# Kernel optimization log

Measured on AMD Instinct MI355X. Metric: run time of the kernel, lower is better.

The kernel has to match this reference:

```python
import jax, jax.numpy as jnp
import numpy as np

BITS = 4
MAXQ = 15          # (1 << BITS) - 1
PACK = 32 // BITS  # 8 values packed per int32


def dequantize(qweight, qzeros, scales, g_idx):
    """GPTQ 4-bit dequant. qweight: [K//8, N] int32, qzeros: [G, N//8] int32,
    scales: [G, N] float, g_idx: [K] int32 -> dense W [K, N] float."""
    N = qweight.shape[1]
    shifts = (jnp.arange(PACK, dtype=jnp.uint32) * BITS)  # [8]
    qw = qweight.astype(jnp.uint32)
    # unpack along K: k = row*8 + j  (matches shifter = (k % 8) * bits)
    w_int = ((qw[:, None, :] >> shifts[None, :, None]) & MAXQ).reshape(-1, N)  # [K, N]
    qz = qzeros.astype(jnp.uint32)
    # unpack along N: n = col*8 + j  (matches zeros_shifter = (n % 8) * bits)
    z_int = ((qz[:, :, None] >> shifts[None, None, :]) & MAXQ).reshape(qzeros.shape[0], -1) + 1  # [G, N]
    dt = scales.dtype
    # group-wise dequant: w = (q - zero) * scale, gathered per-row via g_idx
    return (w_int.astype(dt) - z_int[g_idx].astype(dt)) * scales[g_idx]


def setup_inputs() -> dict:
    key = jax.random.key(0)
    k1, k2, k3, k4, k5 = jax.random.split(key, 5)
    M, K, N, GS = 128, 4096, 11008, 128
    G = K // GS
    x = jax.random.normal(k1, (M, K), dtype=jnp.float32)
    qweight = jax.random.randint(k2, (K // PACK, N), 0, 2147483647, dtype=jnp.int32)
    qzeros = jax.random.randint(k3, (G, N // PACK), 0, 2147483647, dtype=jnp.int32)
    scales = jax.random.uniform(k4, (G, N), dtype=jnp.float32, minval=0.001, maxval=0.01)
    bias = jax.random.normal(k5, (N,), dtype=jnp.float32)
    g_idx = (jnp.arange(K, dtype=jnp.int32) // GS).astype(jnp.int32)
    return {"x": x, "qweight": qweight, "qzeros": qzeros, "scales": scales,
            "bias": bias, "g_idx": g_idx}


def reference(x, qweight, qzeros, scales, bias, g_idx):
    w = dequantize(qweight, qzeros, scales, g_idx)  # [K, N]
    return x @ w + bias
```

## Files before the change

kernel.cpp:

```cpp
#include <hip/hip_runtime.h>
#include <stdint.h>


#define M_DIM 128
#define K_DIM 4096
#define N_DIM 11008
#define GS    128
#define NG    32
#define SPLIT 4
#define GPB   (NG / SPLIT)
#define PART_STRIDE ((size_t)M_DIM * N_DIM)

typedef _Float16 half8  __attribute__((ext_vector_type(8)));
typedef _Float16 half2t __attribute__((ext_vector_type(2)));
typedef _Float16 half4t __attribute__((ext_vector_type(4)));
typedef float    f32x4  __attribute__((ext_vector_type(4)));

__global__ void k_prep(const float* __restrict__ x, const int* __restrict__ qzeros,
                       const float* __restrict__ scales,
                       _Float16* __restrict__ xh, float* __restrict__ zs) {
    int b = blockIdx.x, tid = threadIdx.x;
    if (b < 512) {
        int i = (b * 256 + tid) * 4;
        float4 v = *(const float4*)(x + i);
        half4t o;
        o[0] = (_Float16)v.x; o[1] = (_Float16)v.y;
        o[2] = (_Float16)v.z; o[3] = (_Float16)v.w;
        *(half4t*)(xh + i) = o;
    } else {
        b -= 512;
        int g = b / 43;
        int n = (b - g * 43) * 256 + tid;
        unsigned qz = (unsigned)qzeros[g * (N_DIM / 8) + (n >> 3)];
        float z = (float)((qz >> ((n & 7) * 4)) & 15u) + 1.0f;
        zs[g * N_DIM + n] = z * scales[g * N_DIM + n];
    }
}

__device__ __forceinline__ void load_lds16(const void* g, void* l) {
    __builtin_amdgcn_global_load_lds(
        (const __attribute__((address_space(1))) unsigned int*)g,
        (__attribute__((address_space(3))) unsigned int*)l, 16, 0, 0);
}

__device__ __forceinline__ half8 dequant8(unsigned q, half2t S2, half2t Z2) {
    const half2t BIAS = __builtin_bit_cast(half2t, 0x64006400u);
    half2t w[4];
#pragma unroll
    for (int p = 0; p < 4; ++p) {
        unsigned r = __builtin_amdgcn_perm(q, q, 0x00010001u * (unsigned)p);
        unsigned t = (r & 0x00F0000Fu) | 0x64006400u;
        w[p] = __builtin_elementwise_fma(__builtin_bit_cast(half2t, t) - BIAS, S2, Z2);
    }
    half4t lo = __builtin_shufflevector(w[0], w[1], 0, 1, 2, 3);
    half4t hi = __builtin_shufflevector(w[2], w[3], 0, 1, 2, 3);
    return __builtin_shufflevector(lo, hi, 0, 1, 2, 3, 4, 5, 6, 7);
}

__global__ __launch_bounds__(512, 4)
void k_gemm(const _Float16* __restrict__ xh,
            const int*      __restrict__ qweight,
            const float*    __restrict__ scales,
            const float*    __restrict__ zst,
            float*          __restrict__ part)
{
    __shared__ _Float16 As[2][128 * 128];

    const int tid  = threadIdx.x;
    const int lane = tid & 63;
    const int w    = tid >> 6;
    const int wx   = w & 1;
    const int wy   = (w >> 1) & 1;
    const int kh   = w >> 2;
    const int q    = lane >> 4;
    const int lr   = lane & 15;

    const int n0 = blockIdx.x * 64;
    const int g0 = blockIdx.y * GPB;
    int ncol[2] = { n0 + wx * 32 + lr, n0 + wx * 32 + lr + 16 };

    f32x4 acc[4][2];
#pragma unroll
    for (int f = 0; f < 4; ++f)
#pragma unroll
        for (int h = 0; h < 2; ++h)
            acc[f][h] = (f32x4){0.f, 0.f, 0.f, 0.f};

    int cm[4], ckb[4];
#pragma unroll
    for (int it = 0; it < 4; ++it) {
        int c = it * 512 + tid;
        cm[it]  = c >> 4;
        ckb[it] = (c & 15) ^ (cm[it] & 15);
    }
    const int wave_lds = w * 64 * 8;

#pragma unroll
    for (int it = 0; it < 4; ++it)
        load_lds16(xh + (size_t)cm[it] * K_DIM + g0 * GS + ckb[it] * 8,
                   &As[0][it * 512 * 8 + wave_lds]);
    unsigned qwn[4];
    float scn[2], zcn[2];
#pragma unroll
    for (int t = 0; t < 2; ++t)
#pragma unroll
        for (int h = 0; h < 2; ++h)
            qwn[t * 2 + h] = (unsigned)qweight[(size_t)(g0 * 16 + (kh * 2 + t) * 4 + q) * N_DIM + ncol[h]];
#pragma unroll
    for (int h = 0; h < 2; ++h) {
        scn[h] = scales[(size_t)g0 * N_DIM + ncol[h]];
        zcn[h] = zst[(size_t)g0 * N_DIM + ncol[h]];
    }

    int p = 0;
    for (int g = 0; g < GPB; ++g) {
        unsigned qw[4];
        float sc[2], zc[2];
#pragma unroll
        for (int i = 0; i < 4; ++i) qw[i] = qwn[i];
#pragma unroll
        for (int h = 0; h < 2; ++h) { sc[h] = scn[h]; zc[h] = zcn[h]; }

        __syncthreads();

        if (g + 1 < GPB) {
            int gn = g0 + g + 1;
#pragma unroll
            for (int it = 0; it < 4; ++it)
                load_lds16(xh + (size_t)cm[it] * K_DIM + gn * GS + ckb[it] * 8,
                           &As[p ^ 1][it * 512 * 8 + wave_lds]);
#pragma unroll
            for (int t = 0; t < 2; ++t)
#pragma unroll
                for (int h = 0; h < 2; ++h)
                    qwn[t * 2 + h] = (unsigned)qweight[(size_t)(gn * 16 + (kh * 2 + t) * 4 + q) * N_DIM + ncol[h]];
#pragma unroll
            for (int h = 0; h < 2; ++h) {
                scn[h] = scales[(size_t)gn * N_DIM + ncol[h]];
                zcn[h] = zst[(size_t)gn * N_DIM + ncol[h]];
            }
        }

        half2t S2[2], Z2[2];
#pragma unroll
        for (int h = 0; h < 2; ++h) {
            float s = sc[h], z1 = zc[h];
            S2[h][0] = (_Float16)s;
            S2[h][1] = (_Float16)(s * 0.0625f);
            Z2[h][0] = (_Float16)(-z1);
            Z2[h][1] = (_Float16)(-z1);
        }

#pragma unroll
        for (int t = 0; t < 2; ++t) {
            const int kk = kh * 2 + t;
            half8 bf[2];
#pragma unroll
            for (int h = 0; h < 2; ++h)
                bf[h] = dequant8(qw[t * 2 + h], S2[h], Z2[h]);
#pragma unroll
            for (int f = 0; f < 4; ++f) {
                int m   = wy * 64 + f * 16 + lr;
                int kb2 = (kk * 4 + q) ^ lr;
                half8 af = *(const half8*)(&As[p][m * 128 + kb2 * 8]);
#pragma unroll
                for (int h = 0; h < 2; ++h)
                    acc[f][h] = __builtin_amdgcn_mfma_f32_16x16x32_f16(af, bf[h], acc[f][h], 0, 0, 0);
            }
        }
        p ^= 1;
    }

    __syncthreads();
    float* red = (float*)&As[0][0];
    const int pid = w & 3;
    if (w >= 4) {
#pragma unroll
        for (int f = 0; f < 4; ++f)
#pragma unroll
            for (int h = 0; h < 2; ++h)
                *(f32x4*)(red + pid * 2048 + (f * 2 + h) * 256 + lane * 4) = acc[f][h];
    }
    __syncthreads();
    if (w < 4) {
        float* po = part + (size_t)blockIdx.y * PART_STRIDE;
#pragma unroll
        for (int f = 0; f < 4; ++f) {
            int mrow = wy * 64 + f * 16 + q * 4;
#pragma unroll
            for (int h = 0; h < 2; ++h) {
                f32x4 o = acc[f][h] + *(const f32x4*)(red + pid * 2048 + (f * 2 + h) * 256 + lane * 4);
#pragma unroll
                for (int r = 0; r < 4; ++r)
                    po[(size_t)(mrow + r) * N_DIM + ncol[h]] = o[r];
            }
        }
    }
}

__global__ void k_reduce(const float* __restrict__ part, const float* __restrict__ bias,
                         float* __restrict__ out) {
    int i = (blockIdx.x * 256 + threadIdx.x) * 4;
    int m = i / N_DIM;
    int n = i - m * N_DIM;
    f32x4 s = *(const f32x4*)(bias + n);
#pragma unroll
    for (int sp = 0; sp < SPLIT; ++sp)
        s += *(const f32x4*)(part + sp * PART_STRIDE + i);
    *(f32x4*)(out + i) = s;
}

extern "C" void kernel_launch(void* const* d_in, const int* in_sizes, int n_in,
                              void* d_out, int out_size, void* d_ws, size_t ws_size,
                              hipStream_t stream) {
    const float* x       = (const float*)d_in[0];
    const int*   qweight = (const int*)d_in[1];
    const int*   qzeros  = (const int*)d_in[2];
    const float* scales  = (const float*)d_in[3];
    const float* bias    = (const float*)d_in[4];

    char* ws = (char*)d_ws;
    _Float16* xh   = (_Float16*)ws;
    float*    zst  = (float*)(ws + 1048576);
    float*    part = (float*)(ws + 1048576 + 1409024);

    k_prep  <<<dim3(1888),            dim3(256), 0, stream>>>(x, qzeros, scales, xh, zst);
    k_gemm  <<<dim3(N_DIM/64, SPLIT), dim3(512), 0, stream>>>(xh, qweight, scales, zst, part);
    k_reduce<<<dim3(1376),            dim3(256), 0, stream>>>(part, bias, (float*)d_out);
}
```

Before: 106.5 us.

## Pack fp16 scale/zero pairs and store split-K partials as fp16 fragment tiles

The prep kernel now writes one packed half4 per column holding scale, scale/16 and the negated zero*scale. This replaces the two separate fp32 scale and zero loads in the GEMM with a single 8-byte load and removes the in-loop conversions. Split-K partials are stored in fp16 in MFMA fragment order with contiguous half4 writes rather than scattered fp32 row stores. The reduce kernel reads that layout and does the row scatter itself. Partial traffic is halved, but the rounding of partial sums to fp16 costs accuracy.

```diff
diff --git a/kernel.cpp b/kernel.cpp
--- a/kernel.cpp
+++ b/kernel.cpp
@@ -9,7 +9,8 @@
 #define NG    32
 #define SPLIT 4
 #define GPB   (NG / SPLIT)
-#define PART_STRIDE ((size_t)M_DIM * N_DIM)
+#define NB    (N_DIM / 64)
+#define PART_ELEMS ((size_t)NB * 4 * 2048)
 
 typedef _Float16 half8  __attribute__((ext_vector_type(8)));
 typedef _Float16 half2t __attribute__((ext_vector_type(2)));
@@ -18,7 +19,7 @@
 
 __global__ void k_prep(const float* __restrict__ x, const int* __restrict__ qzeros,
                        const float* __restrict__ scales,
-                       _Float16* __restrict__ xh, float* __restrict__ zs) {
+                       _Float16* __restrict__ xh, _Float16* __restrict__ szp) {
     int b = blockIdx.x, tid = threadIdx.x;
     if (b < 512) {
         int i = (b * 256 + tid) * 4;
@@ -32,8 +33,14 @@
         int g = b / 43;
         int n = (b - g * 43) * 256 + tid;
         unsigned qz = (unsigned)qzeros[g * (N_DIM / 8) + (n >> 3)];
-        float z = (float)((qz >> ((n & 7) * 4)) & 15u) + 1.0f;
-        zs[g * N_DIM + n] = z * scales[g * N_DIM + n];
+        float s  = scales[g * N_DIM + n];
+        float z1 = (float)((qz >> ((n & 7) * 4)) & 15u) + 1.0f;
+        half4t o;
+        o[0] = (_Float16)s;
+        o[1] = (_Float16)(s * 0.0625f);
+        o[2] = (_Float16)(-(z1 * s));
+        o[3] = o[2];
+        *(half4t*)(szp + (size_t)(g * N_DIM + n) * 4) = o;
     }
 }
 
@@ -60,9 +67,8 @@
 __global__ __launch_bounds__(512, 4)
 void k_gemm(const _Float16* __restrict__ xh,
             const int*      __restrict__ qweight,
-            const float*    __restrict__ scales,
-            const float*    __restrict__ zst,
-            float*          __restrict__ part)
+            const _Float16* __restrict__ szp,
+            _Float16*       __restrict__ part)
 {
     __shared__ _Float16 As[2][128 * 128];
 
@@ -100,26 +106,24 @@
         load_lds16(xh + (size_t)cm[it] * K_DIM + g0 * GS + ckb[it] * 8,
                    &As[0][it * 512 * 8 + wave_lds]);
     unsigned qwn[4];
-    float scn[2], zcn[2];
+    half4t   szn[2];
 #pragma unroll
     for (int t = 0; t < 2; ++t)
 #pragma unroll
         for (int h = 0; h < 2; ++h)
             qwn[t * 2 + h] = (unsigned)qweight[(size_t)(g0 * 16 + (kh * 2 + t) * 4 + q) * N_DIM + ncol[h]];
 #pragma unroll
-    for (int h = 0; h < 2; ++h) {
-        scn[h] = scales[(size_t)g0 * N_DIM + ncol[h]];
-        zcn[h] = zst[(size_t)g0 * N_DIM + ncol[h]];
-    }
+    for (int h = 0; h < 2; ++h)
+        szn[h] = *(const half4t*)(szp + ((size_t)g0 * N_DIM + ncol[h]) * 4);
 
     int p = 0;
     for (int g = 0; g < GPB; ++g) {
         unsigned qw[4];
-        float sc[2], zc[2];
+        half4t   sz[2];
 #pragma unroll
         for (int i = 0; i < 4; ++i) qw[i] = qwn[i];
 #pragma unroll
-        for (int h = 0; h < 2; ++h) { sc[h] = scn[h]; zc[h] = zcn[h]; }
+        for (int h = 0; h < 2; ++h) sz[h] = szn[h];
 
         __syncthreads();
 
@@ -135,20 +139,15 @@
                 for (int h = 0; h < 2; ++h)
                     qwn[t * 2 + h] = (unsigned)qweight[(size_t)(gn * 16 + (kh * 2 + t) * 4 + q) * N_DIM + ncol[h]];
 #pragma unroll
-            for (int h = 0; h < 2; ++h) {
-                scn[h] = scales[(size_t)gn * N_DIM + ncol[h]];
-                zcn[h] = zst[(size_t)gn * N_DIM + ncol[h]];
-            }
+            for (int h = 0; h < 2; ++h)
+                szn[h] = *(const half4t*)(szp + ((size_t)gn * N_DIM + ncol[h]) * 4);
         }
 
         half2t S2[2], Z2[2];
 #pragma unroll
         for (int h = 0; h < 2; ++h) {
-            float s = sc[h], z1 = zc[h];
-            S2[h][0] = (_Float16)s;
-            S2[h][1] = (_Float16)(s * 0.0625f);
-            Z2[h][0] = (_Float16)(-z1);
-            Z2[h][1] = (_Float16)(-z1);
+            S2[h] = __builtin_shufflevector(sz[h], sz[h], 0, 1);
+            Z2[h] = __builtin_shufflevector(sz[h], sz[h], 2, 3);
         }
 
 #pragma unroll
@@ -183,31 +182,41 @@
     }
     __syncthreads();
     if (w < 4) {
-        float* po = part + (size_t)blockIdx.y * PART_STRIDE;
+        _Float16* ph = part + (size_t)blockIdx.y * PART_ELEMS
+                     + (size_t)(blockIdx.x * 4 + pid) * 2048;
 #pragma unroll
         for (int f = 0; f < 4; ++f) {
-            int mrow = wy * 64 + f * 16 + q * 4;
 #pragma unroll
             for (int h = 0; h < 2; ++h) {
                 f32x4 o = acc[f][h] + *(const f32x4*)(red + pid * 2048 + (f * 2 + h) * 256 + lane * 4);
-#pragma unroll
-                for (int r = 0; r < 4; ++r)
-                    po[(size_t)(mrow + r) * N_DIM + ncol[h]] = o[r];
+                half4t ov;
+#pragma unroll
+                for (int r = 0; r < 4; ++r) ov[r] = (_Float16)o[r];
+                *(half4t*)(ph + ((f * 2 + h) * 64 + lane) * 4) = ov;
             }
         }
     }
 }
 
-__global__ void k_reduce(const float* __restrict__ part, const float* __restrict__ bias,
+__global__ void k_reduce(const _Float16* __restrict__ part, const float* __restrict__ bias,
                          float* __restrict__ out) {
-    int i = (blockIdx.x * 256 + threadIdx.x) * 4;
-    int m = i / N_DIM;
-    int n = i - m * N_DIM;
-    f32x4 s = *(const f32x4*)(bias + n);
-#pragma unroll
-    for (int sp = 0; sp < SPLIT; ++sp)
-        s += *(const f32x4*)(part + sp * PART_STRIDE + i);
-    *(f32x4*)(out + i) = s;
+    int t = blockIdx.x * 256 + threadIdx.x;
+    int lane = t & 63, fh = (t >> 6) & 7, pid = (t >> 9) & 3, nb = t >> 11;
+    int f = fh >> 1, h = fh & 1, wy = pid >> 1, wx = pid & 1;
+    int q = lane >> 4, lr = lane & 15;
+    int m0 = wy * 64 + f * 16 + q * 4;
+    int n  = nb * 64 + wx * 32 + h * 16 + lr;
+    f32x4 sv = (f32x4){0.f, 0.f, 0.f, 0.f};
+#pragma unroll
+    for (int s = 0; s < SPLIT; ++s) {
+        half4t v = *(const half4t*)(part + s * PART_ELEMS + (size_t)t * 4);
+#pragma unroll
+        for (int r = 0; r < 4; ++r) sv[r] += (float)v[r];
+    }
+    float b = bias[n];
+#pragma unroll
+    for (int r = 0; r < 4; ++r)
+        out[(size_t)(m0 + r) * N_DIM + n] = sv[r] + b;
 }
 
 extern "C" void kernel_launch(void* const* d_in, const int* in_sizes, int n_in,
@@ -221,10 +230,10 @@
 
     char* ws = (char*)d_ws;
     _Float16* xh   = (_Float16*)ws;
-    float*    zst  = (float*)(ws + 1048576);
-    float*    part = (float*)(ws + 1048576 + 1409024);
-
-    k_prep  <<<dim3(1888),            dim3(256), 0, stream>>>(x, qzeros, scales, xh, zst);
-    k_gemm  <<<dim3(N_DIM/64, SPLIT), dim3(512), 0, stream>>>(xh, qweight, scales, zst, part);
-    k_reduce<<<dim3(1376),            dim3(256), 0, stream>>>(part, bias, (float*)d_out);
-}
+    _Float16* szp  = (_Float16*)(ws + 1048576);
+    _Float16* part = (_Float16*)(ws + 1048576 + 2818048);
+
+    k_prep  <<<dim3(1888),         dim3(256), 0, stream>>>(x, qzeros, scales, xh, szp);
+    k_gemm  <<<dim3(NB, SPLIT),    dim3(512), 0, stream>>>(xh, qweight, szp, part);
+    k_reduce<<<dim3(1376),         dim3(256), 0, stream>>>(part, bias, (float*)d_out);
+}
```

Result: no change. 105.0 us (-1.4%).
